# Kernel tuning notes

Measured on AMD Instinct MI355X. Metric: run time of the kernel, lower is better.

The kernel has to match this reference:

```python
import jax, jax.numpy as jnp
import numpy as np

THRESH = 0.7
MIN_KEPT_FRAC = 0.5  # max(0.001, 0.5)
LOG_CLAMP = -100.0   # torch BCELoss clamps log terms at -100


def setup_inputs() -> dict:
    key = jax.random.key(0)
    k1, k2 = jax.random.split(key)
    shape = (32, 1, 1024, 1024)
    pred = jax.random.uniform(k1, shape, dtype=jnp.float32, minval=1e-6, maxval=1.0 - 1e-6)
    target = jnp.round(jax.random.uniform(k2, shape, dtype=jnp.float32))  # binary mask
    return {"pred": pred, "target": target}


def reference(pred, target):
    p = pred.reshape(-1)
    t = target.reshape(-1)
    # elementwise BCE with reduction='none' (torch clamps log at -100)
    log_p = jnp.clip(jnp.log(p), LOG_CLAMP, None)
    log_1mp = jnp.clip(jnp.log1p(-p), LOG_CLAMP, None)
    pixel_losses = -(t * log_p + (1.0 - t) * log_1mp)

    n = p.shape[0]
    min_kept = min(int(MIN_KEPT_FRAC * (n - 1)), n - 1)  # static python int
    p_sorted = jnp.sort(p)
    min_value = p_sorted[min_kept]
    threshold = jnp.maximum(min_value, jnp.float32(THRESH))

    # keeping losses whose pred value is below the threshold; mean over kept
    mask = p < threshold
    cnt = jnp.sum(mask).astype(pixel_losses.dtype)
    return jnp.sum(jnp.where(mask, pixel_losses, 0.0)) / cnt
```

## Files before the change

### kernel.cpp

```cpp
#include <hip/hip_runtime.h>

#define THRESH   0.7f
#define BASEU    0x3F333334u
#define NBINS    2048
#define NSUB     4096
#define NTHREADS 256
#define F4_PER_CHUNK 4096
#define MAXBLK   8192
#define NBLK_FB  1024

struct Blk { float sum_lt, sum_eq; unsigned cnt_lt, cnt_eq; };

struct Ws {
  Blk      blk[MAXBLK];
  double   sum_lt, sum_eq, prefix_sum;
  unsigned cnt_lt, cnt_eq;
  unsigned done;
  unsigned fin0, fin1, fin2, fin3;
  unsigned selBin, rank_r, prefix_cnt;
  unsigned Hcnt[NBINS];
  float    Hsum[NBINS];
  unsigned subCnt[NSUB];
  float    subSum[NSUB];
};

__device__ __forceinline__ float bce_loss(float p, float t) {
  float x = (t > 0.5f) ? p : (1.0f - p);
  return fminf(-__logf(x), 100.0f);
}

__global__ __launch_bounds__(NTHREADS, 4) void k_main(
    const float4* __restrict__ p4, const float4* __restrict__ t4,
    Ws* __restrict__ ws, int n, int nchunks) {
  const int nvec = n >> 2;
  float s_lt = 0.f, s_eq = 0.f;
  unsigned c_lt = 0u, c_eq = 0u;

#define CONSUME(PR, TR)                                                        \
  _Pragma("unroll") for (int j = 0; j < 4; ++j) {                              \
    float pa[4] = {PR[j].x, PR[j].y, PR[j].z, PR[j].w};                        \
    float ta[4] = {TR[j].x, TR[j].y, TR[j].z, TR[j].w};                        \
    _Pragma("unroll") for (int c = 0; c < 4; ++c) {                            \
      float pv = pa[c];                                                        \
      float x  = (ta[c] > 0.5f) ? pv : (1.0f - pv);                            \
      float l  = fminf(-__logf(x), 100.0f);                                    \
      bool lt  = (pv < THRESH);                                                \
      s_lt += lt ? l : 0.0f;                                                   \
      c_lt += lt ? 1u : 0u;                                                    \
      if (__any(pv == THRESH)) {               \
        bool eq = (pv == THRESH);                                              \
        c_eq += eq ? 1u : 0u;                                                  \
        s_eq += eq ? l : 0.0f;                                                 \
      }                                                                        \
    }                                                                          \
  }
#define LOADB(PR, TR, IT)                                                      \
  _Pragma("unroll") for (int j = 0; j < 4; ++j) {                              \
    PR[j] = pp[(IT) * 1024 + j * 256];                                         \
    TR[j] = tt[(IT) * 1024 + j * 256];                                         \
  }

  for (int chunk = blockIdx.x; chunk < nchunks; chunk += gridDim.x) {
    const int start = chunk * F4_PER_CHUNK;
    if (start + F4_PER_CHUNK <= nvec) {
      const float4* pp = p4 + start + threadIdx.x;
      const float4* tt = t4 + start + threadIdx.x;
      float4 pA[4], tA[4], pB[4], tB[4];
      LOADB(pA, tA, 0)
      LOADB(pB, tB, 1)
      CONSUME(pA, tA)
      LOADB(pA, tA, 2)
      CONSUME(pB, tB)
      LOADB(pB, tB, 3)
      CONSUME(pA, tA)
      CONSUME(pB, tB)
    } else {
      int lim = start + F4_PER_CHUNK; if (lim > nvec) lim = nvec;
      for (int f = start + threadIdx.x; f < lim; f += NTHREADS) {
        float4 p = p4[f];
        float4 t = t4[f];
        float pa[4] = {p.x, p.y, p.z, p.w};
        float ta[4] = {t.x, t.y, t.z, t.w};
#pragma unroll
        for (int c = 0; c < 4; ++c) {
          float pv = pa[c];
          float l = bce_loss(pv, ta[c]);
          if (pv < THRESH)       { c_lt++; s_lt += l; }
          else if (pv == THRESH) { c_eq++; s_eq += l; }
        }
      }
    }
  }
#undef LOADB
#undef CONSUME
  if (blockIdx.x == 0) {
    int i = (nvec << 2) + threadIdx.x;
    if (i < n) {
      float pv = ((const float*)p4)[i];
      float l = bce_loss(pv, ((const float*)t4)[i]);
      if (pv < THRESH)       { c_lt++; s_lt += l; }
      else if (pv == THRESH) { c_eq++; s_eq += l; }
    }
  }

#pragma unroll
  for (int off = 32; off > 0; off >>= 1) {
    s_lt += __shfl_down(s_lt, off);
    s_eq += __shfl_down(s_eq, off);
    c_lt += __shfl_down(c_lt, off);
    c_eq += __shfl_down(c_eq, off);
  }
  __shared__ float    red_slt[4], red_seq[4];
  __shared__ unsigned red_clt[4], red_ceq[4];
  int wave = threadIdx.x >> 6;
  if ((threadIdx.x & 63) == 0) {
    red_slt[wave] = s_lt; red_seq[wave] = s_eq;
    red_clt[wave] = c_lt; red_ceq[wave] = c_eq;
  }
  __syncthreads();
  if (threadIdx.x == 0) {
    Blk b;
    b.sum_lt = red_slt[0] + red_slt[1] + red_slt[2] + red_slt[3];
    b.sum_eq = red_seq[0] + red_seq[1] + red_seq[2] + red_seq[3];
    b.cnt_lt = red_clt[0] + red_clt[1] + red_clt[2] + red_clt[3];
    b.cnt_eq = red_ceq[0] + red_ceq[1] + red_ceq[2] + red_ceq[3];
    ws->blk[blockIdx.x] = b;
  }
}

__global__ __launch_bounds__(1024) void k_decide(
    float* __restrict__ out, Ws* __restrict__ ws, int nblk, int kidx) {
  double s_lt = 0.0, s_eq = 0.0;
  unsigned long long c_lt = 0, c_eq = 0;
  for (int i = threadIdx.x; i < nblk; i += 1024) {
    Blk b = ws->blk[i];
    s_lt += (double)b.sum_lt; s_eq += (double)b.sum_eq;
    c_lt += b.cnt_lt;         c_eq += b.cnt_eq;
  }
#pragma unroll
  for (int off = 32; off > 0; off >>= 1) {
    s_lt += __shfl_down(s_lt, off);
    s_eq += __shfl_down(s_eq, off);
    c_lt += __shfl_down(c_lt, off);
    c_eq += __shfl_down(c_eq, off);
  }
  __shared__ double rs[16], rq[16];
  __shared__ unsigned long long rc[16], re[16];
  int wave = threadIdx.x >> 6;
  if ((threadIdx.x & 63) == 0) { rs[wave] = s_lt; rq[wave] = s_eq; rc[wave] = c_lt; re[wave] = c_eq; }
  __syncthreads();
  if (threadIdx.x == 0) {
    double slt = 0.0, seq = 0.0; unsigned long long clt = 0, ceq = 0;
    for (int w = 0; w < 16; ++w) { slt += rs[w]; seq += rq[w]; clt += rc[w]; ceq += re[w]; }
    ws->sum_lt = slt; ws->sum_eq = seq;
    ws->cnt_lt = (unsigned)clt; ws->cnt_eq = (unsigned)ceq;
    ws->fin0 = 0u; ws->fin1 = 0u; ws->fin2 = 0u; ws->fin3 = 0u;
    if (clt + ceq > (unsigned long long)kidx) {
      out[0] = (float)(slt / (double)clt);
      ws->done = 1u;
    } else {
      ws->done = 0u;
    }
  }
}

__device__ void gsync(unsigned* ctr, unsigned goal) {
  __syncthreads();
  if (threadIdx.x == 0) {
    __threadfence();
    atomicAdd(ctr, 1u);
    while (atomicAdd(ctr, 0u) < goal) __builtin_amdgcn_s_sleep(8);
  }
  __syncthreads();
  __threadfence();
}

__global__ __launch_bounds__(NTHREADS) void k_fallback(
    const float* __restrict__ pred, const float* __restrict__ targ,
    float* __restrict__ out, Ws* __restrict__ ws, int n, int kidx) {
  if (ws->done) return;

  __shared__ union {
    struct { unsigned hc[NBINS]; float hs[NBINS]; } l1;
    struct { unsigned sc[NSUB];  float ss[NSUB];  } l2;
  } sh;

  const int gtid = blockIdx.x * NTHREADS + threadIdx.x;
  const int gstride = gridDim.x * NTHREADS;

  for (int i = gtid; i < NBINS; i += gstride) { ws->Hcnt[i] = 0u; ws->Hsum[i] = 0.f; }
  for (int i = gtid; i < NSUB;  i += gstride) { ws->subCnt[i] = 0u; ws->subSum[i] = 0.f; }
  gsync(&ws->fin0, gridDim.x);

  for (int i = threadIdx.x; i < NBINS; i += NTHREADS) { sh.l1.hc[i] = 0u; sh.l1.hs[i] = 0.f; }
  __syncthreads();
  for (int i = gtid; i < n; i += gstride) {
    float pv = pred[i];
    if (pv > THRESH) {
      unsigned b = (__float_as_uint(pv) - BASEU) >> 12;
      if (b > NBINS - 1) b = NBINS - 1;
      atomicAdd(&sh.l1.hc[b], 1u);
      atomicAdd(&sh.l1.hs[b], bce_loss(pv, targ[i]));
    }
  }
  __syncthreads();
  for (int i = threadIdx.x; i < NBINS; i += NTHREADS) {
    if (sh.l1.hc[i])        atomicAdd(&ws->Hcnt[i], sh.l1.hc[i]);
    if (sh.l1.hs[i] != 0.f) atomicAdd(&ws->Hsum[i], sh.l1.hs[i]);
  }
  gsync(&ws->fin1, gridDim.x);

  if (blockIdx.x == 0 && threadIdx.x == 0) {
    unsigned long long cum = (unsigned long long)ws->cnt_lt + ws->cnt_eq;
    double csum = ws->sum_lt + ws->sum_eq;
    for (int b = 0; b < NBINS; ++b) {
      unsigned hcnt = atomicAdd(&ws->Hcnt[b], 0u);
      if (cum + hcnt > (unsigned long long)kidx) {
        atomicExch(&ws->selBin, (unsigned)b);
        atomicExch(&ws->rank_r, (unsigned)((unsigned long long)kidx - cum));
        atomicExch(&ws->prefix_cnt, (unsigned)cum);
        ws->prefix_sum = csum;
        break;
      }
      cum  += hcnt;
      csum += (double)atomicAdd(&ws->Hsum[b], 0.f);
    }
  }
  gsync(&ws->fin2, gridDim.x);

  unsigned base = BASEU + (atomicAdd(&ws->selBin, 0u) << 12);
  for (int i = threadIdx.x; i < NSUB; i += NTHREADS) { sh.l2.sc[i] = 0u; sh.l2.ss[i] = 0.f; }
  __syncthreads();
  for (int i = gtid; i < n; i += gstride) {
    unsigned u = __float_as_uint(pred[i]);
    if (u >= base && u < base + NSUB) {
      atomicAdd(&sh.l2.sc[u - base], 1u);
      atomicAdd(&sh.l2.ss[u - base], bce_loss(pred[i], targ[i]));
    }
  }
  __syncthreads();
  for (int i = threadIdx.x; i < NSUB; i += NTHREADS) {
    if (sh.l2.sc[i])         atomicAdd(&ws->subCnt[i], sh.l2.sc[i]);
    if (sh.l2.ss[i] != 0.f)  atomicAdd(&ws->subSum[i], sh.l2.ss[i]);
  }
  gsync(&ws->fin3, gridDim.x);

  if (blockIdx.x == 0 && threadIdx.x == 0) {
    unsigned r = atomicAdd(&ws->rank_r, 0u);
    unsigned long long cum = 0;
    double csum = 0.0;
    for (int i = 0; i < NSUB; ++i) {
      unsigned c = atomicAdd(&ws->subCnt[i], 0u);
      if (cum + c > (unsigned long long)r) {
        unsigned long long cnt_final = (unsigned long long)atomicAdd(&ws->prefix_cnt, 0u) + cum;
        double sum_final = ws->prefix_sum + csum;
        out[0] = (float)(sum_final / (double)cnt_final);
        break;
      }
      cum  += c;
      csum += (double)atomicAdd(&ws->subSum[i], 0.f);
    }
  }
}

extern "C" void kernel_launch(void* const* d_in, const int* in_sizes, int n_in,
                              void* d_out, int out_size, void* d_ws, size_t ws_size,
                              hipStream_t stream) {
  const float* pred = (const float*)d_in[0];
  const float* targ = (const float*)d_in[1];
  float* out = (float*)d_out;
  Ws* ws = (Ws*)d_ws;
  int n = in_sizes[0];
  long long kll = (long long)(n - 1) / 2;
  if (kll > (long long)(n - 1)) kll = n - 1;
  int kidx = (int)kll;

  int nvec = n >> 2;
  int nchunks = (nvec + F4_PER_CHUNK - 1) / F4_PER_CHUNK;
  if (nchunks < 1) nchunks = 1;
  int nblk = nchunks > MAXBLK ? MAXBLK : nchunks;

  k_main    <<<nblk, NTHREADS, 0, stream>>>((const float4*)pred, (const float4*)targ, ws, n, nchunks);
  k_decide  <<<1, 1024, 0, stream>>>(out, ws, nblk, kidx);
  k_fallback<<<NBLK_FB, NTHREADS, 0, stream>>>(pred, targ, out, ws, n, kidx);
}
```

Baseline: 283.2 us.

## Replace chunked double-buffered main loop with simple grid-stride float4 loop

Removes the per-block 4096-float4 chunk loop with explicit double-buffered register loads and the wave-vote guarded equality branch. Each thread now walks a plain grid-stride loop over float4s and computes the less-than and equal accumulations branchlessly. The grid is sized to nvec/256 capped at 8192 blocks, so each thread handles about four float4s, and the launch-bounds occupancy hint is dropped. The aim is simpler code with more blocks in flight, at the cost of less explicit memory-level parallelism per thread.

```diff
diff --git a/kernel.cpp b/kernel.cpp
--- a/kernel.cpp
+++ b/kernel.cpp
@@ -5,7 +5,6 @@
 #define NBINS    2048
 #define NSUB     4096
 #define NTHREADS 256
-#define F4_PER_CHUNK 4096
 #define MAXBLK   8192
 #define NBLK_FB  1024
 
@@ -29,72 +28,36 @@
   return fminf(-__logf(x), 100.0f);
 }
 
-__global__ __launch_bounds__(NTHREADS, 4) void k_main(
+__global__ void k_main(
     const float4* __restrict__ p4, const float4* __restrict__ t4,
-    Ws* __restrict__ ws, int n, int nchunks) {
+    Ws* __restrict__ ws, int n) {
   const int nvec = n >> 2;
+  const int tid = blockIdx.x * NTHREADS + threadIdx.x;
+  const int stride = gridDim.x * NTHREADS;
+
   float s_lt = 0.f, s_eq = 0.f;
   unsigned c_lt = 0u, c_eq = 0u;
 
-#define CONSUME(PR, TR)                                                        \
-  _Pragma("unroll") for (int j = 0; j < 4; ++j) {                              \
-    float pa[4] = {PR[j].x, PR[j].y, PR[j].z, PR[j].w};                        \
-    float ta[4] = {TR[j].x, TR[j].y, TR[j].z, TR[j].w};                        \
-    _Pragma("unroll") for (int c = 0; c < 4; ++c) {                            \
-      float pv = pa[c];                                                        \
-      float x  = (ta[c] > 0.5f) ? pv : (1.0f - pv);                            \
-      float l  = fminf(-__logf(x), 100.0f);                                    \
-      bool lt  = (pv < THRESH);                                                \
-      s_lt += lt ? l : 0.0f;                                                   \
-      c_lt += lt ? 1u : 0u;                                                    \
-      if (__any(pv == THRESH)) {               \
-        bool eq = (pv == THRESH);                                              \
-        c_eq += eq ? 1u : 0u;                                                  \
-        s_eq += eq ? l : 0.0f;                                                 \
-      }                                                                        \
-    }                                                                          \
-  }
-#define LOADB(PR, TR, IT)                                                      \
-  _Pragma("unroll") for (int j = 0; j < 4; ++j) {                              \
-    PR[j] = pp[(IT) * 1024 + j * 256];                                         \
-    TR[j] = tt[(IT) * 1024 + j * 256];                                         \
-  }
-
-  for (int chunk = blockIdx.x; chunk < nchunks; chunk += gridDim.x) {
-    const int start = chunk * F4_PER_CHUNK;
-    if (start + F4_PER_CHUNK <= nvec) {
-      const float4* pp = p4 + start + threadIdx.x;
-      const float4* tt = t4 + start + threadIdx.x;
-      float4 pA[4], tA[4], pB[4], tB[4];
-      LOADB(pA, tA, 0)
-      LOADB(pB, tB, 1)
-      CONSUME(pA, tA)
-      LOADB(pA, tA, 2)
-      CONSUME(pB, tB)
-      LOADB(pB, tB, 3)
-      CONSUME(pA, tA)
-      CONSUME(pB, tB)
-    } else {
-      int lim = start + F4_PER_CHUNK; if (lim > nvec) lim = nvec;
-      for (int f = start + threadIdx.x; f < lim; f += NTHREADS) {
-        float4 p = p4[f];
-        float4 t = t4[f];
-        float pa[4] = {p.x, p.y, p.z, p.w};
-        float ta[4] = {t.x, t.y, t.z, t.w};
+  for (int i = tid; i < nvec; i += stride) {
+    float4 p = p4[i];
+    float4 t = t4[i];
+    float pa[4] = {p.x, p.y, p.z, p.w};
+    float ta[4] = {t.x, t.y, t.z, t.w};
 #pragma unroll
-        for (int c = 0; c < 4; ++c) {
-          float pv = pa[c];
-          float l = bce_loss(pv, ta[c]);
-          if (pv < THRESH)       { c_lt++; s_lt += l; }
-          else if (pv == THRESH) { c_eq++; s_eq += l; }
-        }
-      }
-    }
-  }
-#undef LOADB
-#undef CONSUME
-  if (blockIdx.x == 0) {
-    int i = (nvec << 2) + threadIdx.x;
+    for (int c = 0; c < 4; ++c) {
+      float pv = pa[c];
+      float x  = (ta[c] > 0.5f) ? pv : (1.0f - pv);
+      float l  = fminf(-__logf(x), 100.0f);
+      bool lt  = (pv <  THRESH);
+      bool eq  = (pv == THRESH);
+      s_lt += lt ? l : 0.0f;
+      c_lt += lt ? 1u : 0u;
+      s_eq += eq ? l : 0.0f;
+      c_eq += eq ? 1u : 0u;
+    }
+  }
+  {
+    int i = (nvec << 2) + tid;
     if (i < n) {
       float pv = ((const float*)p4)[i];
       float l = bce_loss(pv, ((const float*)t4)[i]);
@@ -276,11 +239,11 @@
   int kidx = (int)kll;
 
   int nvec = n >> 2;
-  int nchunks = (nvec + F4_PER_CHUNK - 1) / F4_PER_CHUNK;
-  if (nchunks < 1) nchunks = 1;
-  int nblk = nchunks > MAXBLK ? MAXBLK : nchunks;
-
-  k_main    <<<nblk, NTHREADS, 0, stream>>>((const float4*)pred, (const float4*)targ, ws, n, nchunks);
+  int nblk = (nvec + NTHREADS - 1) / NTHREADS;
+  if (nblk > MAXBLK) nblk = MAXBLK;
+  if (nblk < 1) nblk = 1;
+
+  k_main    <<<nblk, NTHREADS, 0, stream>>>((const float4*)pred, (const float4*)targ, ws, n);
   k_decide  <<<1, 1024, 0, stream>>>(out, ws, nblk, kidx);
   k_fallback<<<NBLK_FB, NTHREADS, 0, stream>>>(pred, targ, out, ws, n, kidx);
 }
```

Result: faster. 275.5 us (-2.7%).
